# Kernel tuning notes

Measured on AMD Instinct MI355X. Metric: run time of the kernel, lower is better.

The kernel has to match this reference:

```python
import jax, jax.numpy as jnp
import numpy as np

B = 32768      # batch
S = 512        # state_dim
G = 128        # goal_dim
A = 32         # action_dim
P = 16         # num_primitives
H1, H2 = 512, 256        # big_model hidden sizes
VH1, VH2 = 1024, 512     # value hidden sizes


def _w(k, shape, scale=0.05):
    return jax.random.normal(k, shape, jnp.float32) * scale


def setup_inputs() -> dict:
    key = jax.random.key(0)
    ks = jax.random.split(key, 24)
    d = {"features": jax.random.normal(ks[0], (B, S + G), jnp.float32)}
    # state encoder: S->H1->H2
    d["se_w1"] = _w(ks[1], (S, H1));  d["se_b1"] = jnp.zeros((H1,), jnp.float32)
    d["se_w2"] = _w(ks[2], (H1, H2)); d["se_b2"] = jnp.zeros((H2,), jnp.float32)
    # goal encoder: G->H1->H2
    d["ge_w1"] = _w(ks[3], (G, H1));  d["ge_b1"] = jnp.zeros((H1,), jnp.float32)
    d["ge_w2"] = _w(ks[4], (H1, H2)); d["ge_b2"] = jnp.zeros((H2,), jnp.float32)
    # gate: 2*H2->H2->P (sigmoid)
    d["gt_w1"] = _w(ks[5], (2 * H2, H2)); d["gt_b1"] = jnp.zeros((H2,), jnp.float32)
    d["gt_w2"] = _w(ks[6], (H2, P));      d["gt_b2"] = jnp.zeros((P,), jnp.float32)
    # primitive state encoder: S->H1->H2
    d["pse_w1"] = _w(ks[7], (S, H1));  d["pse_b1"] = jnp.zeros((H1,), jnp.float32)
    d["pse_w2"] = _w(ks[8], (H1, H2)); d["pse_b2"] = jnp.zeros((H2,), jnp.float32)
    # P primitives, each H2->H2->2A (stacked for batched GEMM)
    d["pw1"] = _w(ks[9], (P, H2, H2));     d["pb1"] = jnp.zeros((P, H2), jnp.float32)
    d["pw2"] = _w(ks[10], (P, H2, 2 * A)); d["pb2"] = jnp.zeros((P, 2 * A), jnp.float32)
    # value net: (S+G)->VH1->VH2
    d["vf_w1"] = _w(ks[11], (S + G, VH1)); d["vf_b1"] = jnp.zeros((VH1,), jnp.float32)
    d["vf_w2"] = _w(ks[12], (VH1, VH2));   d["vf_b2"] = jnp.zeros((VH2,), jnp.float32)
    return d


def _mlp2(x, w1, b1, w2, b2):
    return jax.nn.relu(jax.nn.relu(x @ w1 + b1) @ w2 + b2)


def reference(features,
              se_w1, se_b1, se_w2, se_b2,
              ge_w1, ge_b1, ge_w2, ge_b2,
              gt_w1, gt_b1, gt_w2, gt_b2,
              pse_w1, pse_b1, pse_w2, pse_b2,
              pw1, pb1, pw2, pb2,
              vf_w1, vf_b1, vf_w2, vf_b2):
    state, goal = features[:, :S], features[:, S:]
    # gating weights
    s_emb = _mlp2(state, se_w1, se_b1, se_w2, se_b2)      # [B,H2]
    g_emb = _mlp2(goal, ge_w1, ge_b1, ge_w2, ge_b2)       # [B,H2]
    gate_in = jnp.concatenate([s_emb, g_emb], axis=-1)    # [B,2*H2]
    weights = jax.nn.sigmoid(jax.nn.relu(gate_in @ gt_w1 + gt_b1) @ gt_w2 + gt_b2)  # [B,P]
    # shared primitive embedding
    prim_embed = _mlp2(state, pse_w1, pse_b1, pse_w2, pse_b2)  # [B,H2]
    # all primitives as one batched GEMM
    h = jax.nn.relu(jnp.einsum('bh,phk->bpk', prim_embed, pw1) + pb1[None])  # [B,P,H2]
    out = jnp.einsum('bpk,pkd->bpd', h, pw2) + pb2[None]                      # [B,P,2A]
    mu, log_std = out[..., :A], out[..., A:]
    sigma = jnp.exp(log_std)
    # precision-weighted Gaussian mixture
    inv = weights[..., None] / sigma        # [B,P,A]
    denom = inv.sum(axis=1)                 # [B,A]
    mean = (inv * mu).sum(axis=1) / denom   # [B,A]  (learn_log_std=True -> mean only)
    # critic
    value = _mlp2(features, vf_w1, vf_b1, vf_w2, vf_b2)  # [B,VH2]
    return (mean, value)
```

## Files before the change

### kernel.cpp

```cpp
#include <hip/hip_runtime.h>
#include <stdint.h>

#define NB 32768

typedef __bf16 bf16x8 __attribute__((ext_vector_type(8)));
typedef float f32x4 __attribute__((ext_vector_type(4)));

__device__ __forceinline__ unsigned pack_bf2(float a, float b) {
  union { __bf16 h[2]; unsigned u; } t;
  t.h[0] = (__bf16)a; t.h[1] = (__bf16)b;
  return t.u;
}
__device__ __forceinline__ unsigned short bf16b(float f) {
  union { __bf16 h; unsigned short u; } t;
  t.h = (__bf16)f;
  return t.u;
}
__device__ __forceinline__ float bf2f(unsigned short h) {
  union { unsigned u; float f; } v; v.u = ((unsigned)h) << 16;
  return v.f;
}

__device__ __forceinline__ void gld_lds16(void* lds, const void* g) {
  __builtin_amdgcn_global_load_lds(
      (__attribute__((address_space(1))) unsigned int*)(uintptr_t)g,
      (__attribute__((address_space(3))) unsigned int*)(uintptr_t)lds,
      16, 0, 0);
}

__device__ __forceinline__ int xcd_swz(int bid, int nwg) {
  return (bid & 7) * (nwg >> 3) + (bid >> 3);
}


__global__ __launch_bounds__(256) void fconv_k(const float* __restrict__ src,
                                               unsigned short* __restrict__ dst) {
  size_t idx = ((size_t)blockIdx.x * 256 + threadIdx.x) * 8;
  float4 a = *(const float4*)(src + idx);
  float4 b = *(const float4*)(src + idx + 4);
  uint4 o;
  o.x = pack_bf2(a.x, a.y); o.y = pack_bf2(a.z, a.w);
  o.z = pack_bf2(b.x, b.y); o.w = pack_bf2(b.z, b.w);
  *(uint4*)(dst + idx) = o;
}

__global__ __launch_bounds__(256) void bcat_k(const float* __restrict__ a,
                                              const float* __restrict__ b,
                                              float* __restrict__ dst) {
  const int i = blockIdx.x * 256 + threadIdx.x;
  dst[i] = (i < 512) ? a[i] : b[i - 512];
}

struct TJobs {
  const float* src[11];
  unsigned short* dst[11];
  int K[11], N[11], batch[11];
};

__global__ __launch_bounds__(256) void wtrans_k(TJobs jobs) {
  const int job = blockIdx.y;
  const int K = jobs.K[job], N = jobs.N[job];
  const int KT = K >> 5, NT = N >> 5;
  const int ntiles = jobs.batch[job] * KT * NT;
  const int t = blockIdx.x;
  if (t >= ntiles) return;
  const int b = t / (KT * NT);
  const int rem = t - b * KT * NT;
  const int kt = rem / NT, nt = rem - kt * NT;
  const float* src = jobs.src[job] + (size_t)b * K * N;
  unsigned short* dst = jobs.dst[job] + (size_t)b * K * N;
  __shared__ float tile[32][33];
  const int i = threadIdx.x >> 5, jj = threadIdx.x & 31;
#pragma unroll
  for (int s = 0; s < 4; ++s)
    tile[i + 8 * s][jj] = src[(size_t)(kt * 32 + i + 8 * s) * N + nt * 32 + jj];
  __syncthreads();
#pragma unroll
  for (int s = 0; s < 4; ++s)
    dst[(size_t)(nt * 32 + i + 8 * s) * K + kt * 32 + jj] = bf16b(tile[jj][i + 8 * s]);
}


template <bool OUT_BF16>
__device__ __forceinline__ void gemm2_body(const unsigned short* __restrict__ A, int lda,
                                           const unsigned short* __restrict__ WT,
                                           const float* __restrict__ bias,
                                           void* __restrict__ Cout, int ldc, int K,
                                           int ncl2, int bid, int nwg,
                                           unsigned short (*a_s)[128 * 32],
                                           unsigned short (*b_s)[256 * 32]) {
  const int tid = threadIdx.x;
  const int l = tid & 63, w = tid >> 6;
  const int lr = l & 15, lq = l >> 4;
  const int wg = xcd_swz(bid, nwg);
  const int col0 = (wg & ((1 << ncl2) - 1)) << 8;
  const int row0 = (wg >> ncl2) << 7;
  const int wbase = tid & ~63;

  auto stage = [&](int t) {
    const int buf = t % 3;
    const int k0 = t << 5;
#pragma unroll
    for (int i = 0; i < 2; ++i) {
      const int s = i * 256 + tid;
      const int r = s >> 2, c = s & 3;
      const int cs = c ^ ((r >> 1) & 3);
      gld_lds16(&a_s[buf][(size_t)(i * 256 + wbase) * 8],
                A + (size_t)(row0 + r) * lda + k0 + cs * 8);
    }
#pragma unroll
    for (int i = 0; i < 4; ++i) {
      const int s = i * 256 + tid;
      const int n = s >> 2, c = s & 3;
      const int cs = c ^ ((n >> 1) & 3);
      gld_lds16(&b_s[buf][(size_t)(i * 256 + wbase) * 8],
                WT + (size_t)(col0 + n) * K + k0 + cs * 8);
    }
  };

  f32x4 acc[8][4] = {};
  const int nt = K >> 5;
  stage(0);
  stage(1);
#pragma unroll 1
  for (int t = 0; t < nt; ++t) {
    if (t + 1 < nt) asm volatile("s_waitcnt vmcnt(6)" ::: "memory");
    else            asm volatile("s_waitcnt vmcnt(0)" ::: "memory");
    __builtin_amdgcn_s_barrier();
    if (t + 2 < nt) stage(t + 2);
    const int cur = t % 3;
    bf16x8 av[8], bv[4];
#pragma unroll
    for (int mf = 0; mf < 8; ++mf) {
      const int r = mf * 16 + lr;
      av[mf] = *(const bf16x8*)&a_s[cur][r * 32 + ((lq ^ ((r >> 1) & 3)) << 3)];
    }
#pragma unroll
    for (int nf = 0; nf < 4; ++nf) {
      const int n = w * 64 + nf * 16 + lr;
      bv[nf] = *(const bf16x8*)&b_s[cur][n * 32 + ((lq ^ ((n >> 1) & 3)) << 3)];
    }
#pragma unroll
    for (int mf = 0; mf < 8; ++mf)
#pragma unroll
      for (int nf = 0; nf < 4; ++nf)
        acc[mf][nf] = __builtin_amdgcn_mfma_f32_16x16x32_bf16(av[mf], bv[nf], acc[mf][nf], 0, 0, 0);
  }

#pragma unroll
  for (int nf = 0; nf < 4; ++nf) {
    const int gc = col0 + w * 64 + nf * 16 + lr;
    const float bb = bias[gc];
#pragma unroll
    for (int mf = 0; mf < 8; ++mf) {
      const int gr = row0 + mf * 16 + (lq << 2);
#pragma unroll
      for (int r = 0; r < 4; ++r) {
        float v = acc[mf][nf][r] + bb;
        v = fmaxf(v, 0.0f);
        if (OUT_BF16)
          ((unsigned short*)Cout)[(size_t)(gr + r) * ldc + gc] = bf16b(v);
        else
          ((float*)Cout)[(size_t)(gr + r) * ldc + gc] = v;
      }
    }
  }
}

template <bool OUT_BF16>
__global__ __launch_bounds__(256, 2) void gemm2_k(const unsigned short* __restrict__ A, int lda,
                                                  const unsigned short* __restrict__ WT,
                                                  const float* __restrict__ bias,
                                                  void* __restrict__ Cout, int ldc, int K,
                                                  int ncl2) {
  __shared__ unsigned short a_s[3][128 * 32];
  __shared__ unsigned short b_s[3][256 * 32];
  gemm2_body<OUT_BF16>(A, lda, WT, bias, Cout, ldc, K, ncl2,
                       blockIdx.x, gridDim.x, a_s, b_s);
}

__global__ __launch_bounds__(256, 2) void gemm2_dual_k(
    const unsigned short* __restrict__ A0, int lda0,
    const unsigned short* __restrict__ W0, const float* __restrict__ b0,
    unsigned short* __restrict__ C0, int ldc0, int K0, int ncl20, int nwg0,
    const unsigned short* __restrict__ A1, int lda1,
    const unsigned short* __restrict__ W1, const float* __restrict__ b1,
    unsigned short* __restrict__ C1, int ldc1, int K1, int ncl21, int nwg1) {
  __shared__ unsigned short a_s[3][128 * 32];
  __shared__ unsigned short b_s[3][256 * 32];
  if ((int)blockIdx.x < nwg0)
    gemm2_body<true>(A0, lda0, W0, b0, C0, ldc0, K0, ncl20,
                     blockIdx.x, nwg0, a_s, b_s);
  else
    gemm2_body<true>(A1, lda1, W1, b1, C1, ldc1, K1, ncl21,
                     blockIdx.x - nwg0, nwg1, a_s, b_s);
}


__global__ __launch_bounds__(256, 2) void gemm3_dual_k(
    const unsigned short* __restrict__ A0, int lda0,
    const unsigned short* __restrict__ W0, const float* __restrict__ b0,
    unsigned short* __restrict__ C0, int ldc0,
    const unsigned short* __restrict__ A1, int lda1,
    const unsigned short* __restrict__ W1, const float* __restrict__ b1,
    unsigned short* __restrict__ C1, int ldc1) {
  __shared__ unsigned short a_s[3][128 * 32];
  __shared__ unsigned short b_s[3][128 * 32];
  const int tid = threadIdx.x;
  const int l = tid & 63, w = tid >> 6;
  const int wm = w >> 1, wn = w & 1;
  const int lr = l & 15, lq = l >> 4;
  const int job = blockIdx.x >> 9;
  const unsigned short* A  = job ? A1 : A0;
  const unsigned short* WT = job ? W1 : W0;
  const float* bias        = job ? b1 : b0;
  unsigned short* Cout     = job ? C1 : C0;
  const int lda = job ? lda1 : lda0;
  const int ldc = job ? ldc1 : ldc0;
  const int wg = xcd_swz(blockIdx.x & 511, 512);
  const int col0 = (wg & 1) << 7;
  const int row0 = (wg >> 1) << 7;
  const int wbase = tid & ~63;
  const int K = 512;

  auto stage = [&](int t) {
    const int buf = t % 3;
    const int k0 = t << 5;
#pragma unroll
    for (int i = 0; i < 2; ++i) {
      const int s = i * 256 + tid;
      const int r = s >> 2, c = s & 3;
      const int cs = c ^ ((r >> 1) & 3);
      gld_lds16(&a_s[buf][(size_t)(i * 256 + wbase) * 8],
                A + (size_t)(row0 + r) * lda + k0 + cs * 8);
    }
#pragma unroll
    for (int i = 0; i < 2; ++i) {
      const int s = i * 256 + tid;
      const int n = s >> 2, c = s & 3;
      const int cs = c ^ ((n >> 1) & 3);
      gld_lds16(&b_s[buf][(size_t)(i * 256 + wbase) * 8],
                WT + (size_t)(col0 + n) * K + k0 + cs * 8);
    }
  };

  f32x4 acc[4][4] = {};
  const int nt = K >> 5;
  stage(0);
  stage(1);
#pragma unroll 1
  for (int t = 0; t < nt; ++t) {
    if (t + 1 < nt) asm volatile("s_waitcnt vmcnt(4)" ::: "memory");
    else            asm volatile("s_waitcnt vmcnt(0)" ::: "memory");
    __builtin_amdgcn_s_barrier();
    if (t + 2 < nt) stage(t + 2);
    const int cur = t % 3;
    bf16x8 av[4], bv[4];
#pragma unroll
    for (int mf = 0; mf < 4; ++mf) {
      const int r = wm * 64 + mf * 16 + lr;
      av[mf] = *(const bf16x8*)&a_s[cur][r * 32 + ((lq ^ ((r >> 1) & 3)) << 3)];
    }
#pragma unroll
    for (int nf = 0; nf < 4; ++nf) {
      const int n = wn * 64 + nf * 16 + lr;
      bv[nf] = *(const bf16x8*)&b_s[cur][n * 32 + ((lq ^ ((n >> 1) & 3)) << 3)];
    }
#pragma unroll
    for (int mf = 0; mf < 4; ++mf)
#pragma unroll
      for (int nf = 0; nf < 4; ++nf)
        acc[mf][nf] = __builtin_amdgcn_mfma_f32_16x16x32_bf16(av[mf], bv[nf], acc[mf][nf], 0, 0, 0);
  }

#pragma unroll
  for (int nf = 0; nf < 4; ++nf) {
    const int gc = col0 + wn * 64 + nf * 16 + lr;
    const float bb = bias[gc];
#pragma unroll
    for (int mf = 0; mf < 4; ++mf) {
      const int gr = row0 + wm * 64 + mf * 16 + (lq << 2);
#pragma unroll
      for (int r = 0; r < 4; ++r) {
        float v = acc[mf][nf][r] + bb;
        v = fmaxf(v, 0.0f);
        Cout[(size_t)(gr + r) * ldc + gc] = bf16b(v);
      }
    }
  }
}


__global__ __launch_bounds__(256) void gt2_k(const unsigned short* __restrict__ gate_h,
                                             const float* __restrict__ w2,
                                             const float* __restrict__ b2,
                                             float* __restrict__ wgt) {
  __shared__ float w_s[256 * 16];
  __shared__ unsigned short a_s[16 * 264];
  const int tid = threadIdx.x;
  const int row0 = blockIdx.x * 16;
  for (int i = tid; i < 256 * 16; i += 256) w_s[i] = w2[i];
  for (int i = tid; i < 512; i += 256) {
    const int r = i >> 5, cg = i & 31;
    *(uint4*)&a_s[r * 264 + cg * 8] =
        *(const uint4*)(gate_h + (size_t)(row0 + r) * 256 + cg * 8);
  }
  __syncthreads();
  const int rr = tid >> 4, col = tid & 15;
  float sum = b2[col];
#pragma unroll 8
  for (int k = 0; k < 256; ++k)
    sum += bf2f(a_s[rr * 264 + k]) * w_s[k * 16 + col];
  wgt[(size_t)(row0 + rr) * 16 + col] = 1.0f / (1.0f + __expf(-sum));
}


__global__ __launch_bounds__(512, 4) void prim_head_k(
    const unsigned short* __restrict__ prim,
    const float* __restrict__ wgt,
    const unsigned short* __restrict__ pw1t,
    const float* __restrict__ pb1,
    const unsigned short* __restrict__ pw2t,
    const float* __restrict__ pb2,
    float* __restrict__ outbuf)
{
  __shared__ unsigned short prim_s[2][128 * 32];
  __shared__ unsigned short w1_s[2][128 * 32];
  __shared__ unsigned short h_s[128 * 128];
  __shared__ unsigned short pw2_s[64 * 128];
  const int tid = threadIdx.x;
  const int l = tid & 63;
  const int w = tid >> 6;
  const int lr = l & 15, lq = l >> 4;
  const int wn2 = w & 1, wr2 = w >> 1;
  const int row0 = blockIdx.x << 7;
  const int pg = blockIdx.y;
  const int p0 = pg << 3;
  const int wbase = tid & ~63;

  auto stage_ab = [&](const unsigned short* w1p_, int t) {
    const int buf = t & 1;
    const int k0 = (t & 7) << 5;
    const int nb2 = (t >> 3) << 7;
    const int rw = tid >> 2, kc = tid & 3;
    const int kcs = kc ^ ((rw >> 1) & 3);
    gld_lds16(&prim_s[buf][(size_t)wbase * 8],
              prim + (size_t)(row0 + rw) * 256 + k0 + kcs * 8);
    gld_lds16(&w1_s[buf][(size_t)wbase * 8],
              w1p_ + (size_t)(nb2 + rw) * 256 + k0 + kcs * 8);
  };
  auto stage_pw2 = [&](const unsigned short* w2p_, int half) {
    const int nbase = half << 7;
#pragma unroll
    for (int i = 0; i < 2; ++i) {
      const int c = i * 512 + tid;
      const int d = c >> 4, kc = c & 15;
      gld_lds16(&pw2_s[(size_t)(i * 512 + wbase) * 8],
                w2p_ + (size_t)d * 256 + nbase + ((kc ^ (d & 7)) << 3));
    }
  };

  stage_ab(pw1t + (size_t)p0 * 65536, 0);
  stage_pw2(pw2t + (size_t)p0 * 16384, 0);

  f32x4 num[2] = {}, den[2] = {};

#pragma unroll 1
  for (int pi = 0; pi < 8; ++pi) {
    const int p = p0 + pi;
    const unsigned short* w1p = pw1t + (size_t)p * 65536;
    const unsigned short* w2p = pw2t + (size_t)p * 16384;

    f32x4 acc2[2][2] = {};

    for (int half = 0; half < 2; ++half) {
      float4 pb1v[4];
#pragma unroll
      for (int nf = 0; nf < 4; ++nf)
        pb1v[nf] = *(const float4*)(pb1 + p * 256 + (half << 7) + wn2 * 64 + nf * 16 + (lq << 2));

      f32x4 acc1[4][2] = {};
#pragma unroll 1
      for (int ks = 0; ks < 8; ++ks) {
        const int t = (half << 3) + ks;
        const int cur = t & 1;
        asm volatile("s_waitcnt vmcnt(0)" ::: "memory");
        __builtin_amdgcn_s_barrier();
        if (t < 15) stage_ab(w1p, t + 1);
        else if (pi < 7) stage_ab(w1p + 65536, 0);
        bf16x8 av[4], bv[2];
#pragma unroll
        for (int nf = 0; nf < 4; ++nf) {
          const int n = wn2 * 64 + nf * 16 + lr;
          av[nf] = *(const bf16x8*)&w1_s[cur][n * 32 + ((lq ^ ((n >> 1) & 3)) << 3)];
        }
#pragma unroll
        for (int rf = 0; rf < 2; ++rf) {
          const int r = wr2 * 32 + rf * 16 + lr;
          bv[rf] = *(const bf16x8*)&prim_s[cur][r * 32 + ((lq ^ ((r >> 1) & 3)) << 3)];
        }
#pragma unroll
        for (int nf = 0; nf < 4; ++nf)
#pragma unroll
          for (int rf = 0; rf < 2; ++rf)
            acc1[nf][rf] = __builtin_amdgcn_mfma_f32_16x16x32_bf16(av[nf], bv[rf], acc1[nf][rf], 0, 0, 0);
      }

#pragma unroll
      for (int nf = 0; nf < 4; ++nf) {
        const int n0 = wn2 * 64 + nf * 16 + (lq << 2);
        const float4 bb = pb1v[nf];
#pragma unroll
        for (int rf = 0; rf < 2; ++rf) {
          const int row = wr2 * 32 + rf * 16 + lr;
          uint2 pk;
          pk.x = pack_bf2(fmaxf(acc1[nf][rf][0] + bb.x, 0.0f),
                          fmaxf(acc1[nf][rf][1] + bb.y, 0.0f));
          pk.y = pack_bf2(fmaxf(acc1[nf][rf][2] + bb.z, 0.0f),
                          fmaxf(acc1[nf][rf][3] + bb.w, 0.0f));
          *(uint2*)&h_s[row * 128 + (((n0 >> 3) ^ (row & 7)) << 3) + (n0 & 7)] = pk;
        }
      }
      asm volatile("s_waitcnt lgkmcnt(0)" ::: "memory");
      __builtin_amdgcn_s_barrier();

      {
        const int dmu = wn2 * 16;
        const int row_a = wr2 * 32;
#pragma unroll
        for (int kc8 = 0; kc8 < 4; ++kc8) {
          const int slot = ((kc8 << 2) + lq) ^ (lr & 7);
          const bf16x8 amu = *(const bf16x8*)&pw2_s[(dmu + lr) * 128 + (slot << 3)];
          const bf16x8 als = *(const bf16x8*)&pw2_s[(dmu + 32 + lr) * 128 + (slot << 3)];
          const bf16x8 b0 = *(const bf16x8*)&h_s[(row_a + lr) * 128 + (slot << 3)];
          const bf16x8 b1 = *(const bf16x8*)&h_s[(row_a + 16 + lr) * 128 + (slot << 3)];
          acc2[0][0] = __builtin_amdgcn_mfma_f32_16x16x32_bf16(amu, b0, acc2[0][0], 0, 0, 0);
          acc2[0][1] = __builtin_amdgcn_mfma_f32_16x16x32_bf16(als, b0, acc2[0][1], 0, 0, 0);
          acc2[1][0] = __builtin_amdgcn_mfma_f32_16x16x32_bf16(amu, b1, acc2[1][0], 0, 0, 0);
          acc2[1][1] = __builtin_amdgcn_mfma_f32_16x16x32_bf16(als, b1, acc2[1][1], 0, 0, 0);
        }
      }
      asm volatile("s_waitcnt lgkmcnt(0)" ::: "memory");
      __builtin_amdgcn_s_barrier();
      if (half == 0) stage_pw2(w2p, 1);
      else if (pi < 7) stage_pw2(w2p + 16384, 0);
    }

    {
      const int d0 = wn2 * 16 + (lq << 2);
      const int row_a = wr2 * 32;
      const float4 b2mu = *(const float4*)(pb2 + p * 64 + d0);
      const float4 b2ls = *(const float4*)(pb2 + p * 64 + 32 + d0);
      const float wp0 = wgt[(size_t)(row0 + row_a + lr) * 16 + p];
      const float wp1 = wgt[(size_t)(row0 + row_a + 16 + lr) * 16 + p];
#pragma unroll
      for (int s = 0; s < 2; ++s) {
        const float wp = s ? wp1 : wp0;
        const float mu0 = acc2[s][0][0] + b2mu.x, ls0 = acc2[s][1][0] + b2ls.x;
        const float mu1 = acc2[s][0][1] + b2mu.y, ls1 = acc2[s][1][1] + b2ls.y;
        const float mu2 = acc2[s][0][2] + b2mu.z, ls2 = acc2[s][1][2] + b2ls.z;
        const float mu3 = acc2[s][0][3] + b2mu.w, ls3 = acc2[s][1][3] + b2ls.w;
        const float iv0 = wp * __expf(-ls0), iv1 = wp * __expf(-ls1);
        const float iv2 = wp * __expf(-ls2), iv3 = wp * __expf(-ls3);
        num[s][0] += iv0 * mu0; num[s][1] += iv1 * mu1;
        num[s][2] += iv2 * mu2; num[s][3] += iv3 * mu3;
        den[s][0] += iv0; den[s][1] += iv1;
        den[s][2] += iv2; den[s][3] += iv3;
      }
    }
  }

  {
    const int d0 = wn2 * 16 + (lq << 2);
    const int row_a = wr2 * 32;
#pragma unroll
    for (int s = 0; s < 2; ++s) {
      const int row_g = row0 + row_a + s * 16 + lr;
      float* ob = outbuf + ((size_t)row_g * 2 + pg) * 64;
      *(f32x4*)(ob + d0) = num[s];
      *(f32x4*)(ob + 32 + d0) = den[s];
    }
  }
}


__global__ __launch_bounds__(256) void mix_finish_k(const float* __restrict__ buf,
                                                    float* __restrict__ mean_out) {
  const int gid = blockIdx.x * 256 + threadIdx.x;
  const int row = gid >> 3;
  const int a0 = (gid & 7) * 4;
  const float* rp = buf + (size_t)row * 128;
  const f32x4 n0 = *(const f32x4*)(rp + a0);
  const f32x4 d0 = *(const f32x4*)(rp + 32 + a0);
  const f32x4 n1 = *(const f32x4*)(rp + 64 + a0);
  const f32x4 d1 = *(const f32x4*)(rp + 96 + a0);
  f32x4 res;
  res[0] = (n0[0] + n1[0]) / (d0[0] + d1[0]);
  res[1] = (n0[1] + n1[1]) / (d0[1] + d1[1]);
  res[2] = (n0[2] + n1[2]) / (d0[2] + d1[2]);
  res[3] = (n0[3] + n1[3]) / (d0[3] + d1[3]);
  *(f32x4*)(mean_out + (size_t)row * 32 + a0) = res;
}


extern "C" void kernel_launch(void* const* d_in, const int* in_sizes, int n_in,
                              void* d_out, int out_size, void* d_ws, size_t ws_size,
                              hipStream_t stream) {
  const float* features = (const float*)d_in[0];
  const float* se_w1 = (const float*)d_in[1];
  const float* se_b1 = (const float*)d_in[2];
  const float* se_w2 = (const float*)d_in[3];
  const float* se_b2 = (const float*)d_in[4];
  const float* ge_w1 = (const float*)d_in[5];
  const float* ge_b1 = (const float*)d_in[6];
  const float* ge_w2 = (const float*)d_in[7];
  const float* ge_b2 = (const float*)d_in[8];
  const float* gt_w1 = (const float*)d_in[9];
  const float* gt_b1 = (const float*)d_in[10];
  const float* gt_w2 = (const float*)d_in[11];
  const float* gt_b2 = (const float*)d_in[12];
  const float* pse_w1 = (const float*)d_in[13];
  const float* pse_b1 = (const float*)d_in[14];
  const float* pse_w2 = (const float*)d_in[15];
  const float* pse_b2 = (const float*)d_in[16];
  const float* pw1 = (const float*)d_in[17];
  const float* pb1 = (const float*)d_in[18];
  const float* pw2 = (const float*)d_in[19];
  const float* pb2 = (const float*)d_in[20];
  const float* vf_w1 = (const float*)d_in[21];
  const float* vf_b1 = (const float*)d_in[22];
  const float* vf_w2 = (const float*)d_in[23];
  const float* vf_b2 = (const float*)d_in[24];
  (void)in_sizes; (void)n_in; (void)out_size; (void)ws_size;

  char* base = (char*)d_ws;
  size_t off = 0;
  auto alloc = [&](size_t bytes) -> char* {
    char* p = base + off;
    off += (bytes + 255) & ~(size_t)255;
    return p;
  };
  unsigned short* fbf     = (unsigned short*)alloc((size_t)NB * 640 * 2);
  unsigned short* bufA    = (unsigned short*)alloc((size_t)NB * 1024 * 2);
  unsigned short* g1      = (unsigned short*)alloc((size_t)NB * 512 * 2);
  unsigned short* gate_in = (unsigned short*)alloc((size_t)NB * 512 * 2);
  unsigned short* gate_h  = (unsigned short*)alloc((size_t)NB * 256 * 2);
  unsigned short* prim    = (unsigned short*)alloc((size_t)NB * 256 * 2);
  float* wgt              = (float*)alloc((size_t)NB * 16 * 4);
  unsigned short* wcat1t  = (unsigned short*)alloc((size_t)1024 * 512 * 2);
  float* bcat1            = (float*)alloc(1024 * 4);
  unsigned short* se_w2t  = (unsigned short*)alloc(256 * 512 * 2);
  unsigned short* ge_w1t  = (unsigned short*)alloc(512 * 128 * 2);
  unsigned short* ge_w2t  = (unsigned short*)alloc(256 * 512 * 2);
  unsigned short* gt_w1t  = (unsigned short*)alloc(256 * 512 * 2);
  unsigned short* pse_w2t = (unsigned short*)alloc(256 * 512 * 2);
  unsigned short* pw1t    = (unsigned short*)alloc((size_t)16 * 256 * 256 * 2);
  unsigned short* pw2t    = (unsigned short*)alloc((size_t)16 * 64 * 256 * 2);
  unsigned short* vf_w1t  = (unsigned short*)alloc(1024 * 640 * 2);
  unsigned short* vf_w2t  = (unsigned short*)alloc(512 * 1024 * 2);

  unsigned short* se_w1t  = wcat1t;
  unsigned short* pse_w1t = wcat1t + 512 * 512;

  float* outbuf = (float*)bufA;

  float* mean_out = (float*)d_out;
  float* value_out = (float*)d_out + (size_t)NB * 32;

  fconv_k<<<dim3(10240), dim3(256), 0, stream>>>(features, fbf);
  bcat_k<<<dim3(4), dim3(256), 0, stream>>>(se_b1, pse_b1, bcat1);

  TJobs jobs;
  auto setj = [&](int i, const float* s, unsigned short* d, int K, int N, int b) {
    jobs.src[i] = s; jobs.dst[i] = d; jobs.K[i] = K; jobs.N[i] = N; jobs.batch[i] = b;
  };
  setj(0, se_w1, se_w1t, 512, 512, 1);
  setj(1, se_w2, se_w2t, 512, 256, 1);
  setj(2, ge_w1, ge_w1t, 128, 512, 1);
  setj(3, ge_w2, ge_w2t, 512, 256, 1);
  setj(4, gt_w1, gt_w1t, 512, 256, 1);
  setj(5, pse_w1, pse_w1t, 512, 512, 1);
  setj(6, pse_w2, pse_w2t, 512, 256, 1);
  setj(7, pw1, pw1t, 256, 256, 16);
  setj(8, pw2, pw2t, 256, 64, 16);
  setj(9, vf_w1, vf_w1t, 640, 1024, 1);
  setj(10, vf_w2, vf_w2t, 1024, 512, 1);
  wtrans_k<<<dim3(1024, 11), dim3(256), 0, stream>>>(jobs);

  gemm2_dual_k<<<dim3(1536), dim3(256), 0, stream>>>(
      fbf, 640, wcat1t, bcat1, bufA, 1024, 512, 2, 1024,
      fbf + 512, 640, ge_w1t, ge_b1, g1, 512, 128, 1, 512);
  gemm3_dual_k<<<dim3(1024), dim3(256), 0, stream>>>(
      bufA, 1024, se_w2t, se_b2, gate_in, 512,
      g1, 512, ge_w2t, ge_b2, gate_in + 256, 512);
  gemm3_dual_k<<<dim3(1024), dim3(256), 0, stream>>>(
      gate_in, 512, gt_w1t, gt_b1, gate_h, 256,
      bufA + 512, 1024, pse_w2t, pse_b2, prim, 256);
  gt2_k<<<dim3(2048), dim3(256), 0, stream>>>(gate_h, gt_w2, gt_b2, wgt);
  gemm2_k<true><<<dim3(1024), dim3(256), 0, stream>>>(fbf, 640, vf_w1t, vf_b1, bufA, 1024, 640, 2);
  gemm2_k<false><<<dim3(512), dim3(256), 0, stream>>>(bufA, 1024, vf_w2t, vf_b2, value_out, 512, 1024, 1);
  prim_head_k<<<dim3(256, 2), dim3(512), 0, stream>>>(prim, wgt, pw1t, pb1, pw2t, pb2, outbuf);
  mix_finish_k<<<dim3(1024), dim3(256), 0, stream>>>(outbuf, mean_out);
}
```

Measured before the change: 407.8 us.

## Fuse value-head second GEMM and primitive head into one interleaved launch

```diff
diff --git a/kernel.cpp b/kernel.cpp
--- a/kernel.cpp
+++ b/kernel.cpp
@@ -315,170 +315,252 @@
 }
 
 
-__global__ __launch_bounds__(512, 4) void prim_head_k(
-    const unsigned short* __restrict__ prim,
-    const float* __restrict__ wgt,
-    const unsigned short* __restrict__ pw1t,
-    const float* __restrict__ pb1,
-    const unsigned short* __restrict__ pw2t,
-    const float* __restrict__ pb2,
-    float* __restrict__ outbuf)
-{
-  __shared__ unsigned short prim_s[2][128 * 32];
-  __shared__ unsigned short w1_s[2][128 * 32];
-  __shared__ unsigned short h_s[128 * 128];
-  __shared__ unsigned short pw2_s[64 * 128];
+__global__ __launch_bounds__(512, 4) void fused_tail_k(
+    const unsigned short* __restrict__ prim, const float* __restrict__ wgt,
+    const unsigned short* __restrict__ pw1t, const float* __restrict__ pb1,
+    const unsigned short* __restrict__ pw2t, const float* __restrict__ pb2,
+    float* __restrict__ outbuf,
+    const unsigned short* __restrict__ v1, const unsigned short* __restrict__ vf_w2t,
+    const float* __restrict__ vf_b2, float* __restrict__ value_out) {
+  __shared__ char lds_raw[81920];
   const int tid = threadIdx.x;
-  const int l = tid & 63;
-  const int w = tid >> 6;
-  const int lr = l & 15, lq = l >> 4;
-  const int wn2 = w & 1, wr2 = w >> 1;
-  const int row0 = blockIdx.x << 7;
-  const int pg = blockIdx.y;
-  const int p0 = pg << 3;
-  const int wbase = tid & ~63;
-
-  auto stage_ab = [&](const unsigned short* w1p_, int t) {
-    const int buf = t & 1;
-    const int k0 = (t & 7) << 5;
-    const int nb2 = (t >> 3) << 7;
-    const int rw = tid >> 2, kc = tid & 3;
-    const int kcs = kc ^ ((rw >> 1) & 3);
-    gld_lds16(&prim_s[buf][(size_t)wbase * 8],
-              prim + (size_t)(row0 + rw) * 256 + k0 + kcs * 8);
-    gld_lds16(&w1_s[buf][(size_t)wbase * 8],
-              w1p_ + (size_t)(nb2 + rw) * 256 + k0 + kcs * 8);
-  };
-  auto stage_pw2 = [&](const unsigned short* w2p_, int half) {
-    const int nbase = half << 7;
-#pragma unroll
-    for (int i = 0; i < 2; ++i) {
-      const int c = i * 512 + tid;
-      const int d = c >> 4, kc = c & 15;
-      gld_lds16(&pw2_s[(size_t)(i * 512 + wbase) * 8],
-                w2p_ + (size_t)d * 256 + nbase + ((kc ^ (d & 7)) << 3));
-    }
-  };
-
-  stage_ab(pw1t + (size_t)p0 * 65536, 0);
-  stage_pw2(pw2t + (size_t)p0 * 16384, 0);
-
-  f32x4 num[2] = {}, den[2] = {};
+  const int idx = blockIdx.x >> 1;
+
+  if ((blockIdx.x & 1) == 0) {
+    unsigned short (*prim_s)[128 * 32] = (unsigned short (*)[128 * 32])(lds_raw);
+    unsigned short (*w1_s)[128 * 32]   = (unsigned short (*)[128 * 32])(lds_raw + 16384);
+    unsigned short* h_s   = (unsigned short*)(lds_raw + 32768);
+    unsigned short* pw2_s = (unsigned short*)(lds_raw + 65536);
+    const int l = tid & 63;
+    const int w = tid >> 6;
+    const int lr = l & 15, lq = l >> 4;
+    const int wn2 = w & 1, wr2 = w >> 1;
+    const int row0 = (idx & 255) << 7;
+    const int pg = idx >> 8;
+    const int p0 = pg << 3;
+    const int wbase = tid & ~63;
+
+    auto stage_ab = [&](const unsigned short* w1p_, int t) {
+      const int buf = t & 1;
+      const int k0 = (t & 7) << 5;
+      const int nb2 = (t >> 3) << 7;
+      const int rw = tid >> 2, kc = tid & 3;
+      const int kcs = kc ^ ((rw >> 1) & 3);
+      gld_lds16(&prim_s[buf][(size_t)wbase * 8],
+                prim + (size_t)(row0 + rw) * 256 + k0 + kcs * 8);
+      gld_lds16(&w1_s[buf][(size_t)wbase * 8],
+                w1p_ + (size_t)(nb2 + rw) * 256 + k0 + kcs * 8);
+    };
+    auto stage_pw2 = [&](const unsigned short* w2p_, int half) {
+      const int nbase = half << 7;
+#pragma unroll
+      for (int i = 0; i < 2; ++i) {
+        const int c = i * 512 + tid;
+        const int d = c >> 4, kc = c & 15;
+        gld_lds16(&pw2_s[(size_t)(i * 512 + wbase) * 8],
+                  w2p_ + (size_t)d * 256 + nbase + ((kc ^ (d & 7)) << 3));
+      }
+    };
+
+    stage_ab(pw1t + (size_t)p0 * 65536, 0);
+    stage_pw2(pw2t + (size_t)p0 * 16384, 0);
+
+    f32x4 num[2] = {}, den[2] = {};
 
 #pragma unroll 1
-  for (int pi = 0; pi < 8; ++pi) {
-    const int p = p0 + pi;
-    const unsigned short* w1p = pw1t + (size_t)p * 65536;
-    const unsigned short* w2p = pw2t + (size_t)p * 16384;
-
-    f32x4 acc2[2][2] = {};
-
-    for (int half = 0; half < 2; ++half) {
-      float4 pb1v[4];
-#pragma unroll
-      for (int nf = 0; nf < 4; ++nf)
-        pb1v[nf] = *(const float4*)(pb1 + p * 256 + (half << 7) + wn2 * 64 + nf * 16 + (lq << 2));
-
-      f32x4 acc1[4][2] = {};
+    for (int pi = 0; pi < 8; ++pi) {
+      const int p = p0 + pi;
+      const unsigned short* w1p = pw1t + (size_t)p * 65536;
+      const unsigned short* w2p = pw2t + (size_t)p * 16384;
+
+      f32x4 acc2[2][2] = {};
+
+      for (int half = 0; half < 2; ++half) {
+        float4 pb1v[4];
+#pragma unroll
+        for (int nf = 0; nf < 4; ++nf)
+          pb1v[nf] = *(const float4*)(pb1 + p * 256 + (half << 7) + wn2 * 64 + nf * 16 + (lq << 2));
+
+        f32x4 acc1[4][2] = {};
 #pragma unroll 1
-      for (int ks = 0; ks < 8; ++ks) {
-        const int t = (half << 3) + ks;
-        const int cur = t & 1;
-        asm volatile("s_waitcnt vmcnt(0)" ::: "memory");
+        for (int ks = 0; ks < 8; ++ks) {
+          const int t = (half << 3) + ks;
+          const int cur = t & 1;
+          asm volatile("s_waitcnt vmcnt(0)" ::: "memory");
+          __builtin_amdgcn_s_barrier();
+          if (t < 15) stage_ab(w1p, t + 1);
+          else if (pi < 7) stage_ab(w1p + 65536, 0);
+          bf16x8 av[4], bv[2];
+#pragma unroll
+          for (int nf = 0; nf < 4; ++nf) {
+            const int n = wn2 * 64 + nf * 16 + lr;
+            av[nf] = *(const bf16x8*)&w1_s[cur][n * 32 + ((lq ^ ((n >> 1) & 3)) << 3)];
+          }
+#pragma unroll
+          for (int rf = 0; rf < 2; ++rf) {
+            const int r = wr2 * 32 + rf * 16 + lr;
+            bv[rf] = *(const bf16x8*)&prim_s[cur][r * 32 + ((lq ^ ((r >> 1) & 3)) << 3)];
+          }
+#pragma unroll
+          for (int nf = 0; nf < 4; ++nf)
+#pragma unroll
+            for (int rf = 0; rf < 2; ++rf)
+              acc1[nf][rf] = __builtin_amdgcn_mfma_f32_16x16x32_bf16(av[nf], bv[rf], acc1[nf][rf], 0, 0, 0);
+        }
+
+#pragma unroll
+        for (int nf = 0; nf < 4; ++nf) {
+          const int n0 = wn2 * 64 + nf * 16 + (lq << 2);
+          const float4 bb = pb1v[nf];
+#pragma unroll
+          for (int rf = 0; rf < 2; ++rf) {
+            const int row = wr2 * 32 + rf * 16 + lr;
+            uint2 pk;
+            pk.x = pack_bf2(fmaxf(acc1[nf][rf][0] + bb.x, 0.0f),
+                            fmaxf(acc1[nf][rf][1] + bb.y, 0.0f));
+            pk.y = pack_bf2(fmaxf(acc1[nf][rf][2] + bb.z, 0.0f),
+                            fmaxf(acc1[nf][rf][3] + bb.w, 0.0f));
+            *(uint2*)&h_s[row * 128 + (((n0 >> 3) ^ (row & 7)) << 3) + (n0 & 7)] = pk;
+          }
+        }
+        asm volatile("s_waitcnt lgkmcnt(0)" ::: "memory");
         __builtin_amdgcn_s_barrier();
-        if (t < 15) stage_ab(w1p, t + 1);
-        else if (pi < 7) stage_ab(w1p + 65536, 0);
-        bf16x8 av[4], bv[2];
-#pragma unroll
-        for (int nf = 0; nf < 4; ++nf) {
-          const int n = wn2 * 64 + nf * 16 + lr;
-          av[nf] = *(const bf16x8*)&w1_s[cur][n * 32 + ((lq ^ ((n >> 1) & 3)) << 3)];
+
+        {
+          const int dmu = wn2 * 16;
+          const int row_a = wr2 * 32;
+#pragma unroll
+          for (int kc8 = 0; kc8 < 4; ++kc8) {
+            const int slot = ((kc8 << 2) + lq) ^ (lr & 7);
+            const bf16x8 amu = *(const bf16x8*)&pw2_s[(dmu + lr) * 128 + (slot << 3)];
+            const bf16x8 als = *(const bf16x8*)&pw2_s[(dmu + 32 + lr) * 128 + (slot << 3)];
+            const bf16x8 b0 = *(const bf16x8*)&h_s[(row_a + lr) * 128 + (slot << 3)];
+            const bf16x8 b1 = *(const bf16x8*)&h_s[(row_a + 16 + lr) * 128 + (slot << 3)];
+            acc2[0][0] = __builtin_amdgcn_mfma_f32_16x16x32_bf16(amu, b0, acc2[0][0], 0, 0, 0);
+            acc2[0][1] = __builtin_amdgcn_mfma_f32_16x16x32_bf16(als, b0, acc2[0][1], 0, 0, 0);
+            acc2[1][0] = __builtin_amdgcn_mfma_f32_16x16x32_bf16(amu, b1, acc2[1][0], 0, 0, 0);
+            acc2[1][1] = __builtin_amdgcn_mfma_f32_16x16x32_bf16(als, b1, acc2[1][1], 0, 0, 0);
+          }
         }
-#pragma unroll
-        for (int rf = 0; rf < 2; ++rf) {
-          const int r = wr2 * 32 + rf * 16 + lr;
-          bv[rf] = *(const bf16x8*)&prim_s[cur][r * 32 + ((lq ^ ((r >> 1) & 3)) << 3)];
+        asm volatile("s_waitcnt lgkmcnt(0)" ::: "memory");
+        __builtin_amdgcn_s_barrier();
+        if (half == 0) stage_pw2(w2p, 1);
+        else if (pi < 7) stage_pw2(w2p + 16384, 0);
+      }
+
+      {
+        const int d0 = wn2 * 16 + (lq << 2);
+        const int row_a = wr2 * 32;
+        const float4 b2mu = *(const float4*)(pb2 + p * 64 + d0);
+        const float4 b2ls = *(const float4*)(pb2 + p * 64 + 32 + d0);
+        const float wp0 = wgt[(size_t)(row0 + row_a + lr) * 16 + p];
+        const float wp1 = wgt[(size_t)(row0 + row_a + 16 + lr) * 16 + p];
+#pragma unroll
+        for (int s = 0; s < 2; ++s) {
+          const float wp = s ? wp1 : wp0;
+          const float mu0 = acc2[s][0][0] + b2mu.x, ls0 = acc2[s][1][0] + b2ls.x;
+          const float mu1 = acc2[s][0][1] + b2mu.y, ls1 = acc2[s][1][1] + b2ls.y;
+          const float mu2 = acc2[s][0][2] + b2mu.z, ls2 = acc2[s][1][2] + b2ls.z;
+          const float mu3 = acc2[s][0][3] + b2mu.w, ls3 = acc2[s][1][3] + b2ls.w;
+          const float iv0 = wp * __expf(-ls0), iv1 = wp * __expf(-ls1);
+          const float iv2 = wp * __expf(-ls2), iv3 = wp * __expf(-ls3);
+          num[s][0] += iv0 * mu0; num[s][1] += iv1 * mu1;
+          num[s][2] += iv2 * mu2; num[s][3] += iv3 * mu3;
+          den[s][0] += iv0; den[s][1] += iv1;
+          den[s][2] += iv2; den[s][3] += iv3;
         }
-#pragma unroll
-        for (int nf = 0; nf < 4; ++nf)
-#pragma unroll
-          for (int rf = 0; rf < 2; ++rf)
-            acc1[nf][rf] = __builtin_amdgcn_mfma_f32_16x16x32_bf16(av[nf], bv[rf], acc1[nf][rf], 0, 0, 0);
-      }
-
-#pragma unroll
-      for (int nf = 0; nf < 4; ++nf) {
-        const int n0 = wn2 * 64 + nf * 16 + (lq << 2);
-        const float4 bb = pb1v[nf];
-#pragma unroll
-        for (int rf = 0; rf < 2; ++rf) {
-          const int row = wr2 * 32 + rf * 16 + lr;
-          uint2 pk;
-          pk.x = pack_bf2(fmaxf(acc1[nf][rf][0] + bb.x, 0.0f),
-                          fmaxf(acc1[nf][rf][1] + bb.y, 0.0f));
-          pk.y = pack_bf2(fmaxf(acc1[nf][rf][2] + bb.z, 0.0f),
-                          fmaxf(acc1[nf][rf][3] + bb.w, 0.0f));
-          *(uint2*)&h_s[row * 128 + (((n0 >> 3) ^ (row & 7)) << 3) + (n0 & 7)] = pk;
-        }
-      }
-      asm volatile("s_waitcnt lgkmcnt(0)" ::: "memory");
-      __builtin_amdgcn_s_barrier();
-
-      {
-        const int dmu = wn2 * 16;
-        const int row_a = wr2 * 32;
-#pragma unroll
-        for (int kc8 = 0; kc8 < 4; ++kc8) {
-          const int slot = ((kc8 << 2) + lq) ^ (lr & 7);
-          const bf16x8 amu = *(const bf16x8*)&pw2_s[(dmu + lr) * 128 + (slot << 3)];
-          const bf16x8 als = *(const bf16x8*)&pw2_s[(dmu + 32 + lr) * 128 + (slot << 3)];
-          const bf16x8 b0 = *(const bf16x8*)&h_s[(row_a + lr) * 128 + (slot << 3)];
-          const bf16x8 b1 = *(const bf16x8*)&h_s[(row_a + 16 + lr) * 128 + (slot << 3)];
-          acc2[0][0] = __builtin_amdgcn_mfma_f32_16x16x32_bf16(amu, b0, acc2[0][0], 0, 0, 0);
-          acc2[0][1] = __builtin_amdgcn_mfma_f32_16x16x32_bf16(als, b0, acc2[0][1], 0, 0, 0);
-          acc2[1][0] = __builtin_amdgcn_mfma_f32_16x16x32_bf16(amu, b1, acc2[1][0], 0, 0, 0);
-          acc2[1][1] = __builtin_amdgcn_mfma_f32_16x16x32_bf16(als, b1, acc2[1][1], 0, 0, 0);
-        }
-      }
-      asm volatile("s_waitcnt lgkmcnt(0)" ::: "memory");
-      __builtin_amdgcn_s_barrier();
-      if (half == 0) stage_pw2(w2p, 1);
-      else if (pi < 7) stage_pw2(w2p + 16384, 0);
+      }
     }
 
     {
       const int d0 = wn2 * 16 + (lq << 2);
       const int row_a = wr2 * 32;
-      const float4 b2mu = *(const float4*)(pb2 + p * 64 + d0);
-      const float4 b2ls = *(const float4*)(pb2 + p * 64 + 32 + d0);
-      const float wp0 = wgt[(size_t)(row0 + row_a + lr) * 16 + p];
-      const float wp1 = wgt[(size_t)(row0 + row_a + 16 + lr) * 16 + p];
 #pragma unroll
       for (int s = 0; s < 2; ++s) {
-        const float wp = s ? wp1 : wp0;
-        const float mu0 = acc2[s][0][0] + b2mu.x, ls0 = acc2[s][1][0] + b2ls.x;
-        const float mu1 = acc2[s][0][1] + b2mu.y, ls1 = acc2[s][1][1] + b2ls.y;
-        const float mu2 = acc2[s][0][2] + b2mu.z, ls2 = acc2[s][1][2] + b2ls.z;
-        const float mu3 = acc2[s][0][3] + b2mu.w, ls3 = acc2[s][1][3] + b2ls.w;
-        const float iv0 = wp * __expf(-ls0), iv1 = wp * __expf(-ls1);
-        const float iv2 = wp * __expf(-ls2), iv3 = wp * __expf(-ls3);
-        num[s][0] += iv0 * mu0; num[s][1] += iv1 * mu1;
-        num[s][2] += iv2 * mu2; num[s][3] += iv3 * mu3;
-        den[s][0] += iv0; den[s][1] += iv1;
-        den[s][2] += iv2; den[s][3] += iv3;
-      }
-    }
-  }
-
-  {
-    const int d0 = wn2 * 16 + (lq << 2);
-    const int row_a = wr2 * 32;
-#pragma unroll
-    for (int s = 0; s < 2; ++s) {
-      const int row_g = row0 + row_a + s * 16 + lr;
-      float* ob = outbuf + ((size_t)row_g * 2 + pg) * 64;
-      *(f32x4*)(ob + d0) = num[s];
-      *(f32x4*)(ob + 32 + d0) = den[s];
+        const int row_g = row0 + row_a + s * 16 + lr;
+        float* ob = outbuf + ((size_t)row_g * 2 + pg) * 64;
+        *(f32x4*)(ob + d0) = num[s];
+        *(f32x4*)(ob + 32 + d0) = den[s];
+      }
+    }
+  } else {
+    unsigned short (*a_s)[128 * 32] = (unsigned short (*)[128 * 32])(lds_raw);
+    unsigned short (*b_s)[256 * 32] = (unsigned short (*)[256 * 32])(lds_raw + 24576);
+    const int l = tid & 63, w = tid >> 6;
+    const int lr = l & 15, lq = l >> 4;
+    const int wg = xcd_swz(idx, 512);
+    const int col0 = (wg & 1) << 8;
+    const int row0 = (wg >> 1) << 7;
+    const int wbase = tid & ~63;
+    const int K = 1024;
+    const unsigned short* A = v1;
+
+    auto stage = [&](int t) {
+      const int buf = t % 3;
+      const int k0 = t << 5;
+      {
+        const int r = tid >> 2, c = tid & 3;
+        const int cs = c ^ ((r >> 1) & 3);
+        gld_lds16(&a_s[buf][(size_t)wbase * 8],
+                  A + (size_t)(row0 + r) * K + k0 + cs * 8);
+      }
+#pragma unroll
+      for (int i = 0; i < 2; ++i) {
+        const int s = i * 512 + tid;
+        const int n = s >> 2, c = s & 3;
+        const int cs = c ^ ((n >> 1) & 3);
+        gld_lds16(&b_s[buf][(size_t)(i * 512 + wbase) * 8],
+                  vf_w2t + (size_t)(col0 + n) * K + k0 + cs * 8);
+      }
+    };
+
+    f32x4 acc[8][2] = {};
+    const int nt = K >> 5;
+    stage(0);
+    stage(1);
+#pragma unroll 1
+    for (int t = 0; t < nt; ++t) {
+      if (t + 1 < nt) asm volatile("s_waitcnt vmcnt(3)" ::: "memory");
+      else            asm volatile("s_waitcnt vmcnt(0)" ::: "memory");
+      __builtin_amdgcn_s_barrier();
+      if (t + 2 < nt) stage(t + 2);
+      const int cur = t % 3;
+      bf16x8 bv[2];
+#pragma unroll
+      for (int nf = 0; nf < 2; ++nf) {
+        const int n = w * 32 + nf * 16 + lr;
+        bv[nf] = *(const bf16x8*)&b_s[cur][n * 32 + ((lq ^ ((n >> 1) & 3)) << 3)];
+      }
+#pragma unroll
+      for (int mh = 0; mh < 2; ++mh) {
+        bf16x8 av[4];
+#pragma unroll
+        for (int j = 0; j < 4; ++j) {
+          const int r = (mh * 4 + j) * 16 + lr;
+          av[j] = *(const bf16x8*)&a_s[cur][r * 32 + ((lq ^ ((r >> 1) & 3)) << 3)];
+        }
+#pragma unroll
+        for (int j = 0; j < 4; ++j)
+#pragma unroll
+          for (int nf = 0; nf < 2; ++nf)
+            acc[mh * 4 + j][nf] = __builtin_amdgcn_mfma_f32_16x16x32_bf16(
+                av[j], bv[nf], acc[mh * 4 + j][nf], 0, 0, 0);
+      }
+    }
+
+#pragma unroll
+    for (int nf = 0; nf < 2; ++nf) {
+      const int gc = col0 + w * 32 + nf * 16 + lr;
+      const float bb = vf_b2[gc];
+#pragma unroll
+      for (int mf = 0; mf < 8; ++mf) {
+        const int gr = row0 + mf * 16 + (lq << 2);
+#pragma unroll
+        for (int r = 0; r < 4; ++r) {
+          float v = acc[mf][nf][r] + bb;
+          value_out[(size_t)(gr + r) * 512 + gc] = fmaxf(v, 0.0f);
+        }
+      }
     }
   }
 }
@@ -562,7 +644,7 @@
   unsigned short* se_w1t  = wcat1t;
   unsigned short* pse_w1t = wcat1t + 512 * 512;
 
-  float* outbuf = (float*)bufA;
+  float* outbuf = (float*)g1;
 
   float* mean_out = (float*)d_out;
   float* value_out = (float*)d_out + (size_t)NB * 32;
@@ -598,7 +680,8 @@
       bufA + 512, 1024, pse_w2t, pse_b2, prim, 256);
   gt2_k<<<dim3(2048), dim3(256), 0, stream>>>(gate_h, gt_w2, gt_b2, wgt);
   gemm2_k<true><<<dim3(1024), dim3(256), 0, stream>>>(fbf, 640, vf_w1t, vf_b1, bufA, 1024, 640, 2);
-  gemm2_k<false><<<dim3(512), dim3(256), 0, stream>>>(bufA, 1024, vf_w2t, vf_b2, value_out, 512, 1024, 1);
-  prim_head_k<<<dim3(256, 2), dim3(512), 0, stream>>>(prim, wgt, pw1t, pb1, pw2t, pb2, outbuf);
+  fused_tail_k<<<dim3(1024), dim3(512), 0, stream>>>(
+      prim, wgt, pw1t, pb1, pw2t, pb2, outbuf,
+      bufA, vf_w2t, vf_b2, value_out);
   mix_finish_k<<<dim3(1024), dim3(256), 0, stream>>>(outbuf, mean_out);
 }
```

New measurement: 479.9 us. +17.7%, slower.
